# Kernel optimization log

Hardware: AMD Instinct MI355X
Metric: run time of the kernel (lower is better)

## Reference

```python
import jax, jax.numpy as jnp
import numpy as np

B, S, D = 4, 2048, 768
H = 12
HD = D // H
SCALE = HD ** -0.5


def setup_inputs() -> dict:
    key = jax.random.key(0)
    ks = jax.random.split(key, 5)
    std = D ** -0.5
    return {
        "hidden_states": jax.random.normal(ks[0], (B, S, D), dtype=jnp.float32),
        "qkv_w": jax.random.normal(ks[1], (3 * D, D), dtype=jnp.float32) * std,
        "qkv_b": jnp.zeros((3 * D,), dtype=jnp.float32),
        "proj_w": jax.random.normal(ks[2], (D, D), dtype=jnp.float32) * std,
        "proj_b": jnp.zeros((D,), dtype=jnp.float32),
    }


def reference(hidden_states, qkv_w, qkv_b, proj_w, proj_b):
    b, s, d = hidden_states.shape
    # fused QKV projection: [b,s,3d] -> [3,b,H,s,hd]
    mixed = hidden_states @ qkv_w.T + qkv_b
    mixed = mixed.reshape(b, s, 3, H, HD).transpose(2, 0, 3, 1, 4)
    q, k, v = mixed[0], mixed[1], mixed[2]
    # naive attention: full [b,H,s,s] score matrix, as in original module
    scores = jnp.einsum("bhqd,bhkd->bhqk", q, k) * SCALE
    probs = jax.nn.softmax(scores, axis=-1)
    ctx = jnp.einsum("bhqk,bhkd->bhqd", probs, v)
    ctx = ctx.transpose(0, 2, 1, 3).reshape(b, s, d)
    out = ctx @ proj_w.T + proj_b
    return out
```

## Files before the change

### kernel.cpp

```cpp
#include <hip/hip_runtime.h>
#include <hip/hip_bf16.h>

using short8   = __attribute__((ext_vector_type(8))) short;
using floatx4  = __attribute__((ext_vector_type(4))) float;
using floatx16 = __attribute__((ext_vector_type(16))) float;

#define KDIM 768
#define QSCALE 0.18033688011112042f
#define N1 (8192 * 768)
#define N2 (2304 * 768)
#define N3 (768 * 768)

__device__ __forceinline__ short f2bf(float f) {
    union { float f; unsigned u; } v; v.f = f;
    unsigned r = v.u + 0x7fffu + ((v.u >> 16) & 1u);
    return (short)(r >> 16);
}

__device__ __forceinline__ unsigned pack2bf(float a, float b) {
    __hip_bfloat162 h = __float22bfloat162_rn(float2{a, b});
    union { __hip_bfloat162 h; unsigned u; } c; c.h = h;
    return c.u;
}

__device__ __forceinline__ float fast_exp2(float x) {
#if __has_builtin(__builtin_amdgcn_exp2f)
    return __builtin_amdgcn_exp2f(x);
#else
    return exp2f(x);
#endif
}

__device__ __forceinline__ void async16(const void* g, void* l) {
    __builtin_amdgcn_global_load_lds((const __attribute__((address_space(1))) void*)g,
                                     (__attribute__((address_space(3))) void*)l, 16, 0, 0);
}

__global__ void cvt_all(const float* __restrict__ a, const float* __restrict__ b,
                        const float* __restrict__ c, short* __restrict__ oa,
                        short* __restrict__ ob, short* __restrict__ oc) {
    int i = (blockIdx.x * blockDim.x + threadIdx.x) * 4;
    const float* src; short* dst;
    if (i < N1)            { src = a + i;            dst = oa + i; }
    else if (i < N1 + N2)  { src = b + (i - N1);     dst = ob + (i - N1); }
    else if (i < N1+N2+N3) { src = c + (i - N1 - N2); dst = oc + (i - N1 - N2); }
    else return;
    float4 v = *(const float4*)src;
    short4 o;
    o.x = f2bf(v.x); o.y = f2bf(v.y); o.z = f2bf(v.z); o.w = f2bf(v.w);
    *(short4*)dst = o;
}

__global__ __launch_bounds__(256) void gemm_qkv(
    const short* __restrict__ X, const short* __restrict__ W,
    const float* __restrict__ bias,
    short* __restrict__ Qb, short* __restrict__ Kb, short* __restrict__ Vb)
{
    __shared__ short As[128 * 32];
    __shared__ short Bs[128 * 32];
    int tid = threadIdx.x;
    int w = tid >> 6, l = tid & 63;
    int lane16 = l & 15, quad = l >> 4;
    int wm = w & 1, wn = w >> 1;
    int m0 = blockIdx.y * 128, n0 = blockIdx.x * 128;

    floatx4 acc[4][4] = {};

    int srow = w * 32 + (l >> 2);
    int scol = (l & 3) * 8;
    const short* Xg = X + (size_t)(m0 + srow) * KDIM + scol;
    const short* Wg = W + (size_t)(n0 + srow) * KDIM + scol;
    short* AsW = As + (w * 32) * 32;
    short* BsW = Bs + (w * 32) * 32;

    for (int kb = 0; kb < KDIM; kb += 32) {
        __syncthreads();
        async16(Xg + kb,              AsW);
        async16(Xg + kb + 16 * KDIM,  AsW + 16 * 32);
        async16(Wg + kb,              BsW);
        async16(Wg + kb + 16 * KDIM,  BsW + 16 * 32);
        __syncthreads();
        short8 a[4], b[4];
#pragma unroll
        for (int mt = 0; mt < 4; mt++) a[mt] = *(const short8*)(As + (wm * 64 + mt * 16 + lane16) * 32 + quad * 8);
#pragma unroll
        for (int nt = 0; nt < 4; nt++) b[nt] = *(const short8*)(Bs + (wn * 64 + nt * 16 + lane16) * 32 + quad * 8);
#pragma unroll
        for (int mt = 0; mt < 4; mt++)
#pragma unroll
            for (int nt = 0; nt < 4; nt++)
                acc[mt][nt] = __builtin_amdgcn_mfma_f32_16x16x32_bf16(a[mt], b[nt], acc[mt][nt], 0, 0, 0);
    }

#pragma unroll
    for (int mt = 0; mt < 4; mt++) {
        int row = m0 + wm * 64 + mt * 16 + quad * 4;
#pragma unroll
        for (int nt = 0; nt < 4; nt++) {
            int col = n0 + wn * 64 + nt * 16 + lane16;
            int qkv = (col >= 1536) ? 2 : ((col >= 768) ? 1 : 0);
            int rem = col - qkv * 768;
            int h = rem >> 6, e = rem & 63;
            short* dst = (qkv == 0) ? Qb : ((qkv == 1) ? Kb : Vb);
            float sc = (qkv == 0) ? (float)QSCALE : 1.0f;
            float bv = bias[col];
#pragma unroll
            for (int r = 0; r < 4; r++) {
                int i  = row + r;
                int b_ = i >> 11, s_ = i & 2047;
                dst[(((size_t)(b_ * 12 + h)) * 2048 + s_) * 64 + e] = f2bf((acc[mt][nt][r] + bv) * sc);
            }
        }
    }
}

__global__ __launch_bounds__(256) void transpose_v(
    const short* __restrict__ Vb, short* __restrict__ Vt)
{
    __shared__ short T[64 * 66];
    int tid = threadIdx.x;
    int s0 = blockIdx.x * 64, bh = blockIdx.y;
    const short* src = Vb + (size_t)bh * 2048 * 64;
    short* dst = Vt + (size_t)bh * 64 * 2048;

#pragma unroll
    for (int i = 0; i < 2; i++) {
        int slot = i * 256 + tid;
        int s_loc = slot >> 3, ec = slot & 7;
        short8 v = *(const short8*)(src + (size_t)(s0 + s_loc) * 64 + ec * 8);
        *(short8*)(T + s_loc * 66 + ec * 8) = v;
    }
    __syncthreads();
#pragma unroll
    for (int i = 0; i < 2; i++) {
        int slot = i * 256 + tid;
        int e_loc = slot >> 3, sc = slot & 7;
        short8 o;
#pragma unroll
        for (int j = 0; j < 8; j++) {
            int p = sc * 8 + j;
            int kp = (p & 0x33) | ((p & 4) << 1) | ((p & 8) >> 1);
            o[j] = T[kp * 66 + e_loc];
        }
        *(short8*)(dst + (size_t)e_loc * 2048 + s0 + sc * 8) = o;
    }
}

__global__ __launch_bounds__(256, 3) void attn(
    const short* __restrict__ Qb, const short* __restrict__ Kb,
    const short* __restrict__ Vt, short* __restrict__ Ctx)
{
    __shared__ short Ks[512 * 8];
    __shared__ short Vs[512 * 8];
    int tid = threadIdx.x, w = tid >> 6, l = tid & 63;
    int l32 = l & 31, half = l >> 5;
    int qt = blockIdx.x, bh = blockIdx.y;
    const short* Qh  = Qb + (size_t)bh * 2048 * 64;
    const short* Kh  = Kb + (size_t)bh * 2048 * 64;
    const short* Vth = Vt + (size_t)bh * 64 * 2048;
    int qbase = qt * 128 + w * 32;

    const short* kSrc[2];
    const short* vSrc[2];
    short* kDst[2];
    short* vDst[2];
#pragma unroll
    for (int i = 0; i < 2; i++) {
        int slot = i * 256 + tid;
        int row = slot >> 3;
        int g = (slot & 7) ^ (row & 7);
        kSrc[i] = Kh + (size_t)row * 64 + g * 8;
        vSrc[i] = Vth + (size_t)row * 2048 + g * 8;
        kDst[i] = Ks + (size_t)(i * 256 + w * 64) * 8;
        vDst[i] = Vs + (size_t)(i * 256 + w * 64) * 8;
    }

    short8 qf[4];
#pragma unroll
    for (int ks = 0; ks < 4; ks++)
        qf[ks] = *(const short8*)(Qh + (size_t)(qbase + l32) * 64 + ks * 16 + half * 8);

    float lsum = 0.f;
    floatx16 acc[2] = {};
    int sw = l32 & 7;

    for (int kt = 0; kt < 32; kt++) {
        __syncthreads();
#pragma unroll
        for (int i = 0; i < 2; i++) {
            async16(kSrc[i] + (size_t)kt * 64 * 64, kDst[i]);
            async16(vSrc[i] + (size_t)kt * 64,      vDst[i]);
        }
        __syncthreads();

        floatx16 s[2];
#pragma unroll
        for (int nt = 0; nt < 2; nt++) {
            floatx16 c = {};
            int rowb = (nt * 32 + l32) * 8;
#pragma unroll
            for (int ks = 0; ks < 4; ks++) {
                short8 kf = *(const short8*)(Ks + (size_t)(rowb + ((ks * 2 + half) ^ sw)) * 8);
                c = __builtin_amdgcn_mfma_f32_32x32x16_bf16(kf, qf[ks], c, 0, 0, 0);
            }
            s[nt] = c;
        }

        union { short8 s8; unsigned u[4]; } pa[4];
#pragma unroll
        for (int nt = 0; nt < 2; nt++)
#pragma unroll
            for (int r = 0; r < 16; r += 2) {
                float p0 = fast_exp2(s[nt][r]);
                float p1 = fast_exp2(s[nt][r + 1]);
                lsum += p0 + p1;
                pa[2 * nt + (r >> 3)].u[(r & 7) >> 1] = pack2bf(p0, p1);
            }

#pragma unroll
        for (int nt = 0; nt < 2; nt++) {
            int rowb = (nt * 32 + l32) * 8;
#pragma unroll
            for (int ks = 0; ks < 4; ks++) {
                short8 vf = *(const short8*)(Vs + (size_t)(rowb + ((ks * 2 + half) ^ sw)) * 8);
                acc[nt] = __builtin_amdgcn_mfma_f32_32x32x16_bf16(pa[ks].s8, vf, acc[nt], 0, 0, 0);
            }
        }
    }

    float denom = lsum + __shfl_xor(lsum, 32);
    float inv_self = 1.0f / denom;

    int b_ = bh / 12, h = bh % 12;
#pragma unroll
    for (int nt = 0; nt < 2; nt++)
#pragma unroll
        for (int r = 0; r < 16; r++) {
            int qloc = (r & 3) + 8 * (r >> 2) + 4 * half;
            float invq = __shfl(inv_self, qloc);
            int q = qbase + qloc;
            int e = nt * 32 + l32;
            Ctx[((size_t)(b_ * 2048 + q)) * 768 + h * 64 + e] = f2bf(acc[nt][r] * invq);
        }
}

__global__ __launch_bounds__(256) void gemm_out(
    const short* __restrict__ Ctx, const short* __restrict__ W,
    const float* __restrict__ bias, float* __restrict__ out)
{
    __shared__ short As[128 * 32];
    __shared__ short Bs[128 * 32];
    int tid = threadIdx.x;
    int w = tid >> 6, l = tid & 63;
    int lane16 = l & 15, quad = l >> 4;
    int wm = w & 1, wn = w >> 1;
    int m0 = blockIdx.y * 128, n0 = blockIdx.x * 128;

    floatx4 acc[4][4] = {};

    int srow = w * 32 + (l >> 2);
    int scol = (l & 3) * 8;
    const short* Xg = Ctx + (size_t)(m0 + srow) * KDIM + scol;
    const short* Wg = W + (size_t)(n0 + srow) * KDIM + scol;
    short* AsW = As + (w * 32) * 32;
    short* BsW = Bs + (w * 32) * 32;

    for (int kb = 0; kb < KDIM; kb += 32) {
        __syncthreads();
        async16(Xg + kb,             AsW);
        async16(Xg + kb + 16 * KDIM, AsW + 16 * 32);
        async16(Wg + kb,             BsW);
        async16(Wg + kb + 16 * KDIM, BsW + 16 * 32);
        __syncthreads();
        short8 a[4], b[4];
#pragma unroll
        for (int mt = 0; mt < 4; mt++) a[mt] = *(const short8*)(As + (wm * 64 + mt * 16 + lane16) * 32 + quad * 8);
#pragma unroll
        for (int nt = 0; nt < 4; nt++) b[nt] = *(const short8*)(Bs + (wn * 64 + nt * 16 + lane16) * 32 + quad * 8);
#pragma unroll
        for (int mt = 0; mt < 4; mt++)
#pragma unroll
            for (int nt = 0; nt < 4; nt++)
                acc[mt][nt] = __builtin_amdgcn_mfma_f32_16x16x32_bf16(a[mt], b[nt], acc[mt][nt], 0, 0, 0);
    }

#pragma unroll
    for (int mt = 0; mt < 4; mt++) {
        int row = m0 + wm * 64 + mt * 16 + quad * 4;
#pragma unroll
        for (int nt = 0; nt < 4; nt++) {
            int col = n0 + wn * 64 + nt * 16 + lane16;
            float bv = bias[col];
#pragma unroll
            for (int r = 0; r < 4; r++)
                out[(size_t)(row + r) * 768 + col] = acc[mt][nt][r] + bv;
        }
    }
}

extern "C" void kernel_launch(void* const* d_in, const int* in_sizes, int n_in,
                              void* d_out, int out_size, void* d_ws, size_t ws_size,
                              hipStream_t stream) {
    const float* hs     = (const float*)d_in[0];
    const float* qkv_w  = (const float*)d_in[1];
    const float* qkv_b  = (const float*)d_in[2];
    const float* proj_w = (const float*)d_in[3];
    const float* proj_b = (const float*)d_in[4];
    float* out = (float*)d_out;

    short* Xb  = (short*)d_ws;
    short* W1b = Xb  + (size_t)8192 * 768;
    short* W2b = W1b + (size_t)2304 * 768;
    short* Qb  = W2b + (size_t)768 * 768;
    short* Kb  = Qb  + (size_t)8192 * 768;
    short* Vb  = Kb  + (size_t)8192 * 768;
    short* Ctx = Vb  + (size_t)8192 * 768;
    short* Vt  = Xb;

    int ntot = (N1 + N2 + N3) / 4;
    cvt_all<<<(ntot + 255) / 256, 256, 0, stream>>>(hs, qkv_w, proj_w, Xb, W1b, W2b);

    gemm_qkv<<<dim3(18, 64), 256, 0, stream>>>(Xb, W1b, qkv_b, Qb, Kb, Vb);
    transpose_v<<<dim3(32, 48), 256, 0, stream>>>(Vb, Vt);
    attn<<<dim3(16, 48), 256, 0, stream>>>(Qb, Kb, Vt, Ctx);
    gemm_out<<<dim3(6, 64), 256, 0, stream>>>(Ctx, W2b, proj_b, out);
}
```

Baseline: 221.8 us.

## Fuse V transpose into QKV GEMM epilogue via LDS staging; shrink out-proj tile

The QKV GEMM epilogue now stages each 128x64 output slice in shared memory and writes Q/K rows with coalesced 16-byte stores, while V is written directly in transposed (permuted) layout. This removes the separate transpose_v kernel and its extra global round trip. The scattered 2-byte epilogue stores are also replaced by vector stores. Separately, the output projection GEMM uses 64-row tiles, doubling the grid to 768 blocks for better CU fill, at the cost of less reuse per block.

```diff
diff --git a/kernel.cpp b/kernel.cpp
--- a/kernel.cpp
+++ b/kernel.cpp
@@ -54,10 +54,13 @@
 __global__ __launch_bounds__(256) void gemm_qkv(
     const short* __restrict__ X, const short* __restrict__ W,
     const float* __restrict__ bias,
-    short* __restrict__ Qb, short* __restrict__ Kb, short* __restrict__ Vb)
+    short* __restrict__ Qb, short* __restrict__ Kb, short* __restrict__ Vt)
 {
-    __shared__ short As[128 * 32];
-    __shared__ short Bs[128 * 32];
+    __shared__ __attribute__((aligned(16))) short SMEM[128 * 72];
+    short* As = SMEM;
+    short* Bs = SMEM + 128 * 32;
+    short* T  = SMEM;
+
     int tid = threadIdx.x;
     int w = tid >> 6, l = tid & 63;
     int lane16 = l & 15, quad = l >> 4;
@@ -92,57 +95,57 @@
                 acc[mt][nt] = __builtin_amdgcn_mfma_f32_16x16x32_bf16(a[mt], b[nt], acc[mt][nt], 0, 0, 0);
     }
 
-#pragma unroll
-    for (int mt = 0; mt < 4; mt++) {
-        int row = m0 + wm * 64 + mt * 16 + quad * 4;
-#pragma unroll
-        for (int nt = 0; nt < 4; nt++) {
-            int col = n0 + wn * 64 + nt * 16 + lane16;
-            int qkv = (col >= 1536) ? 2 : ((col >= 768) ? 1 : 0);
-            int rem = col - qkv * 768;
-            int h = rem >> 6, e = rem & 63;
-            short* dst = (qkv == 0) ? Qb : ((qkv == 1) ? Kb : Vb);
-            float sc = (qkv == 0) ? (float)QSCALE : 1.0f;
-            float bv = bias[col];
-#pragma unroll
-            for (int r = 0; r < 4; r++) {
-                int i  = row + r;
-                int b_ = i >> 11, s_ = i & 2047;
-                dst[(((size_t)(b_ * 12 + h)) * 2048 + s_) * 64 + e] = f2bf((acc[mt][nt][r] + bv) * sc);
-            }
-        }
-    }
-}
-
-__global__ __launch_bounds__(256) void transpose_v(
-    const short* __restrict__ Vb, short* __restrict__ Vt)
-{
-    __shared__ short T[64 * 66];
-    int tid = threadIdx.x;
-    int s0 = blockIdx.x * 64, bh = blockIdx.y;
-    const short* src = Vb + (size_t)bh * 2048 * 64;
-    short* dst = Vt + (size_t)bh * 64 * 2048;
-
-#pragma unroll
-    for (int i = 0; i < 2; i++) {
-        int slot = i * 256 + tid;
-        int s_loc = slot >> 3, ec = slot & 7;
-        short8 v = *(const short8*)(src + (size_t)(s0 + s_loc) * 64 + ec * 8);
-        *(short8*)(T + s_loc * 66 + ec * 8) = v;
-    }
-    __syncthreads();
-#pragma unroll
-    for (int i = 0; i < 2; i++) {
-        int slot = i * 256 + tid;
-        int e_loc = slot >> 3, sc = slot & 7;
-        short8 o;
-#pragma unroll
-        for (int j = 0; j < 8; j++) {
-            int p = sc * 8 + j;
-            int kp = (p & 0x33) | ((p & 4) << 1) | ((p & 8) >> 1);
-            o[j] = T[kp * 66 + e_loc];
-        }
-        *(short8*)(dst + (size_t)e_loc * 2048 + s0 + sc * 8) = o;
+    int b_  = m0 >> 11;
+    int m0s = m0 & 2047;
+#pragma unroll
+    for (int g = 0; g < 2; g++) {
+        __syncthreads();
+        if (wn == g) {
+#pragma unroll
+            for (int mt = 0; mt < 4; mt++)
+#pragma unroll
+                for (int nt = 0; nt < 4; nt++) {
+                    int col = n0 + g * 64 + nt * 16 + lane16;
+                    float sc = (col < 768) ? (float)QSCALE : 1.0f;
+                    float bv = bias[col];
+#pragma unroll
+                    for (int r = 0; r < 4; r++) {
+                        int row = wm * 64 + mt * 16 + quad * 4 + r;
+                        T[row * 72 + nt * 16 + lane16] = f2bf((acc[mt][nt][r] + bv) * sc);
+                    }
+                }
+        }
+        __syncthreads();
+        int col0 = n0 + g * 64;
+        int qkv = (col0 >= 1536) ? 2 : ((col0 >= 768) ? 1 : 0);
+        int h = (col0 - qkv * 768) >> 6;
+        size_t bh = (size_t)(b_ * 12 + h);
+        if (qkv < 2) {
+            short* dst = ((qkv == 0) ? Qb : Kb) + bh * 2048 * 64;
+#pragma unroll
+            for (int u = 0; u < 4; u++) {
+                int unit = u * 256 + tid;
+                int row = unit >> 3, c = unit & 7;
+                short8 v = *(const short8*)(T + row * 72 + c * 8);
+                *(short8*)(dst + (size_t)(m0s + row) * 64 + c * 8) = v;
+            }
+        } else {
+            short* dst = Vt + bh * 64 * 2048;
+#pragma unroll
+            for (int u = 0; u < 4; u++) {
+                int unit = u * 256 + tid;
+                int e = unit >> 4, sc_ = unit & 15;
+                short8 o;
+#pragma unroll
+                for (int j = 0; j < 8; j++) {
+                    int pos = sc_ * 8 + j;
+                    int t = pos >> 6, tp = pos & 63;
+                    int kp = (tp & 0x33) | ((tp & 4) << 1) | ((tp & 8) >> 1);
+                    o[j] = T[(t * 64 + kp) * 72 + e];
+                }
+                *(short8*)(dst + (size_t)e * 2048 + m0s + sc_ * 8) = o;
+            }
+        }
     }
 }
 
@@ -248,48 +251,50 @@
     const short* __restrict__ Ctx, const short* __restrict__ W,
     const float* __restrict__ bias, float* __restrict__ out)
 {
-    __shared__ short As[128 * 32];
+    __shared__ short As[64 * 32];
     __shared__ short Bs[128 * 32];
     int tid = threadIdx.x;
     int w = tid >> 6, l = tid & 63;
     int lane16 = l & 15, quad = l >> 4;
-    int wm = w & 1, wn = w >> 1;
-    int m0 = blockIdx.y * 128, n0 = blockIdx.x * 128;
-
-    floatx4 acc[4][4] = {};
-
-    int srow = w * 32 + (l >> 2);
-    int scol = (l & 3) * 8;
-    const short* Xg = Ctx + (size_t)(m0 + srow) * KDIM + scol;
-    const short* Wg = W + (size_t)(n0 + srow) * KDIM + scol;
-    short* AsW = As + (w * 32) * 32;
-    short* BsW = Bs + (w * 32) * 32;
+    int m0 = blockIdx.y * 64, n0 = blockIdx.x * 128;
+
+    floatx4 acc[4][2] = {};
+
+    const short* XgA = Ctx + (size_t)(m0 + (tid >> 2)) * KDIM + (tid & 3) * 8;
+    short* AsD = As + (size_t)(w * 64) * 8;
+    const short* XgB[2];
+    short* BsD[2];
+#pragma unroll
+    for (int i = 0; i < 2; i++) {
+        int unit = i * 256 + tid;
+        XgB[i] = W + (size_t)(n0 + (unit >> 2)) * KDIM + (unit & 3) * 8;
+        BsD[i] = Bs + (size_t)(i * 256 + w * 64) * 8;
+    }
 
     for (int kb = 0; kb < KDIM; kb += 32) {
         __syncthreads();
-        async16(Xg + kb,             AsW);
-        async16(Xg + kb + 16 * KDIM, AsW + 16 * 32);
-        async16(Wg + kb,             BsW);
-        async16(Wg + kb + 16 * KDIM, BsW + 16 * 32);
-        __syncthreads();
-        short8 a[4], b[4];
-#pragma unroll
-        for (int mt = 0; mt < 4; mt++) a[mt] = *(const short8*)(As + (wm * 64 + mt * 16 + lane16) * 32 + quad * 8);
-#pragma unroll
-        for (int nt = 0; nt < 4; nt++) b[nt] = *(const short8*)(Bs + (wn * 64 + nt * 16 + lane16) * 32 + quad * 8);
+        async16(XgA + kb, AsD);
+        async16(XgB[0] + kb, BsD[0]);
+        async16(XgB[1] + kb, BsD[1]);
+        __syncthreads();
+        short8 a[4], b[2];
+#pragma unroll
+        for (int mt = 0; mt < 4; mt++) a[mt] = *(const short8*)(As + (mt * 16 + lane16) * 32 + quad * 8);
+#pragma unroll
+        for (int nt = 0; nt < 2; nt++) b[nt] = *(const short8*)(Bs + (w * 32 + nt * 16 + lane16) * 32 + quad * 8);
 #pragma unroll
         for (int mt = 0; mt < 4; mt++)
 #pragma unroll
-            for (int nt = 0; nt < 4; nt++)
+            for (int nt = 0; nt < 2; nt++)
                 acc[mt][nt] = __builtin_amdgcn_mfma_f32_16x16x32_bf16(a[mt], b[nt], acc[mt][nt], 0, 0, 0);
     }
 
 #pragma unroll
     for (int mt = 0; mt < 4; mt++) {
-        int row = m0 + wm * 64 + mt * 16 + quad * 4;
-#pragma unroll
-        for (int nt = 0; nt < 4; nt++) {
-            int col = n0 + wn * 64 + nt * 16 + lane16;
+        int row = m0 + mt * 16 + quad * 4;
+#pragma unroll
+        for (int nt = 0; nt < 2; nt++) {
+            int col = n0 + w * 32 + nt * 16 + lane16;
             float bv = bias[col];
 #pragma unroll
             for (int r = 0; r < 4; r++)
@@ -313,15 +318,13 @@
     short* W2b = W1b + (size_t)2304 * 768;
     short* Qb  = W2b + (size_t)768 * 768;
     short* Kb  = Qb  + (size_t)8192 * 768;
-    short* Vb  = Kb  + (size_t)8192 * 768;
-    short* Ctx = Vb  + (size_t)8192 * 768;
-    short* Vt  = Xb;
+    short* Vt  = Kb  + (size_t)8192 * 768;
+    short* Ctx = Vt  + (size_t)8192 * 768;
 
     int ntot = (N1 + N2 + N3) / 4;
     cvt_all<<<(ntot + 255) / 256, 256, 0, stream>>>(hs, qkv_w, proj_w, Xb, W1b, W2b);
 
-    gemm_qkv<<<dim3(18, 64), 256, 0, stream>>>(Xb, W1b, qkv_b, Qb, Kb, Vb);
-    transpose_v<<<dim3(32, 48), 256, 0, stream>>>(Vb, Vt);
+    gemm_qkv<<<dim3(18, 64), 256, 0, stream>>>(Xb, W1b, qkv_b, Qb, Kb, Vt);
     attn<<<dim3(16, 48), 256, 0, stream>>>(Qb, Kb, Vt, Ctx);
-    gemm_out<<<dim3(6, 64), 256, 0, stream>>>(Ctx, W2b, proj_b, out);
-}
+    gemm_out<<<dim3(6, 128), 256, 0, stream>>>(Ctx, W2b, proj_b, out);
+}
```

Result: slower. 232.5 us (+4.8%).

## Double-buffer K/V tiles in attention and shrink output GEMM tile

Applied to the files above, without the earlier changes.

The attention kernel now keeps two LDS buffers for K and V and issues the async loads for the next key tile before computing on the current one, removing the second barrier per iteration so loads overlap with MFMA work. LDS use per block doubles, which may limit occupancy at the requested three blocks per CU. Separately, the output projection GEMM moves from 128x128 to 64x128 tiles with each wave owning a 64x32 slab. This doubles the grid to 768 blocks for better CU fill, at the cost of less operand reuse per block.

```diff
diff --git a/kernel.cpp b/kernel.cpp
--- a/kernel.cpp
+++ b/kernel.cpp
@@ -150,8 +150,8 @@
     const short* __restrict__ Qb, const short* __restrict__ Kb,
     const short* __restrict__ Vt, short* __restrict__ Ctx)
 {
-    __shared__ short Ks[512 * 8];
-    __shared__ short Vs[512 * 8];
+    __shared__ short Ks[2][512 * 8];
+    __shared__ short Vs[2][512 * 8];
     int tid = threadIdx.x, w = tid >> 6, l = tid & 63;
     int l32 = l & 31, half = l >> 5;
     int qt = blockIdx.x, bh = blockIdx.y;
@@ -162,8 +162,8 @@
 
     const short* kSrc[2];
     const short* vSrc[2];
-    short* kDst[2];
-    short* vDst[2];
+    short* kDst[2][2];
+    short* vDst[2][2];
 #pragma unroll
     for (int i = 0; i < 2; i++) {
         int slot = i * 256 + tid;
@@ -171,8 +171,11 @@
         int g = (slot & 7) ^ (row & 7);
         kSrc[i] = Kh + (size_t)row * 64 + g * 8;
         vSrc[i] = Vth + (size_t)row * 2048 + g * 8;
-        kDst[i] = Ks + (size_t)(i * 256 + w * 64) * 8;
-        vDst[i] = Vs + (size_t)(i * 256 + w * 64) * 8;
+#pragma unroll
+        for (int b = 0; b < 2; b++) {
+            kDst[b][i] = &Ks[b][(size_t)(i * 256 + w * 64) * 8];
+            vDst[b][i] = &Vs[b][(size_t)(i * 256 + w * 64) * 8];
+        }
     }
 
     short8 qf[4];
@@ -184,14 +187,25 @@
     floatx16 acc[2] = {};
     int sw = l32 & 7;
 
+#pragma unroll
+    for (int i = 0; i < 2; i++) {
+        async16(kSrc[i], kDst[0][i]);
+        async16(vSrc[i], vDst[0][i]);
+    }
+
     for (int kt = 0; kt < 32; kt++) {
         __syncthreads();
-#pragma unroll
-        for (int i = 0; i < 2; i++) {
-            async16(kSrc[i] + (size_t)kt * 64 * 64, kDst[i]);
-            async16(vSrc[i] + (size_t)kt * 64,      vDst[i]);
-        }
-        __syncthreads();
+        int b = kt & 1;
+        if (kt < 31) {
+            int nb = b ^ 1;
+#pragma unroll
+            for (int i = 0; i < 2; i++) {
+                async16(kSrc[i] + (size_t)(kt + 1) * 64 * 64, kDst[nb][i]);
+                async16(vSrc[i] + (size_t)(kt + 1) * 64,      vDst[nb][i]);
+            }
+        }
+        const short* KsB = Ks[b];
+        const short* VsB = Vs[b];
 
         floatx16 s[2];
 #pragma unroll
@@ -200,7 +214,7 @@
             int rowb = (nt * 32 + l32) * 8;
 #pragma unroll
             for (int ks = 0; ks < 4; ks++) {
-                short8 kf = *(const short8*)(Ks + (size_t)(rowb + ((ks * 2 + half) ^ sw)) * 8);
+                short8 kf = *(const short8*)(KsB + (size_t)(rowb + ((ks * 2 + half) ^ sw)) * 8);
                 c = __builtin_amdgcn_mfma_f32_32x32x16_bf16(kf, qf[ks], c, 0, 0, 0);
             }
             s[nt] = c;
@@ -222,7 +236,7 @@
             int rowb = (nt * 32 + l32) * 8;
 #pragma unroll
             for (int ks = 0; ks < 4; ks++) {
-                short8 vf = *(const short8*)(Vs + (size_t)(rowb + ((ks * 2 + half) ^ sw)) * 8);
+                short8 vf = *(const short8*)(VsB + (size_t)(rowb + ((ks * 2 + half) ^ sw)) * 8);
                 acc[nt] = __builtin_amdgcn_mfma_f32_32x32x16_bf16(pa[ks].s8, vf, acc[nt], 0, 0, 0);
             }
         }
@@ -248,48 +262,50 @@
     const short* __restrict__ Ctx, const short* __restrict__ W,
     const float* __restrict__ bias, float* __restrict__ out)
 {
-    __shared__ short As[128 * 32];
+    __shared__ short As[64 * 32];
     __shared__ short Bs[128 * 32];
     int tid = threadIdx.x;
     int w = tid >> 6, l = tid & 63;
     int lane16 = l & 15, quad = l >> 4;
-    int wm = w & 1, wn = w >> 1;
-    int m0 = blockIdx.y * 128, n0 = blockIdx.x * 128;
-
-    floatx4 acc[4][4] = {};
-
-    int srow = w * 32 + (l >> 2);
-    int scol = (l & 3) * 8;
-    const short* Xg = Ctx + (size_t)(m0 + srow) * KDIM + scol;
-    const short* Wg = W + (size_t)(n0 + srow) * KDIM + scol;
-    short* AsW = As + (w * 32) * 32;
-    short* BsW = Bs + (w * 32) * 32;
+    int m0 = blockIdx.y * 64, n0 = blockIdx.x * 128;
+
+    floatx4 acc[4][2] = {};
+
+    const short* XgA = Ctx + (size_t)(m0 + (tid >> 2)) * KDIM + (tid & 3) * 8;
+    short* AsD = As + (size_t)(w * 64) * 8;
+    const short* XgB[2];
+    short* BsD[2];
+#pragma unroll
+    for (int i = 0; i < 2; i++) {
+        int unit = i * 256 + tid;
+        XgB[i] = W + (size_t)(n0 + (unit >> 2)) * KDIM + (unit & 3) * 8;
+        BsD[i] = Bs + (size_t)(i * 256 + w * 64) * 8;
+    }
 
     for (int kb = 0; kb < KDIM; kb += 32) {
         __syncthreads();
-        async16(Xg + kb,             AsW);
-        async16(Xg + kb + 16 * KDIM, AsW + 16 * 32);
-        async16(Wg + kb,             BsW);
-        async16(Wg + kb + 16 * KDIM, BsW + 16 * 32);
-        __syncthreads();
-        short8 a[4], b[4];
-#pragma unroll
-        for (int mt = 0; mt < 4; mt++) a[mt] = *(const short8*)(As + (wm * 64 + mt * 16 + lane16) * 32 + quad * 8);
-#pragma unroll
-        for (int nt = 0; nt < 4; nt++) b[nt] = *(const short8*)(Bs + (wn * 64 + nt * 16 + lane16) * 32 + quad * 8);
+        async16(XgA + kb, AsD);
+        async16(XgB[0] + kb, BsD[0]);
+        async16(XgB[1] + kb, BsD[1]);
+        __syncthreads();
+        short8 a[4], b[2];
+#pragma unroll
+        for (int mt = 0; mt < 4; mt++) a[mt] = *(const short8*)(As + (mt * 16 + lane16) * 32 + quad * 8);
+#pragma unroll
+        for (int nt = 0; nt < 2; nt++) b[nt] = *(const short8*)(Bs + (w * 32 + nt * 16 + lane16) * 32 + quad * 8);
 #pragma unroll
         for (int mt = 0; mt < 4; mt++)
 #pragma unroll
-            for (int nt = 0; nt < 4; nt++)
+            for (int nt = 0; nt < 2; nt++)
                 acc[mt][nt] = __builtin_amdgcn_mfma_f32_16x16x32_bf16(a[mt], b[nt], acc[mt][nt], 0, 0, 0);
     }
 
 #pragma unroll
     for (int mt = 0; mt < 4; mt++) {
-        int row = m0 + wm * 64 + mt * 16 + quad * 4;
-#pragma unroll
-        for (int nt = 0; nt < 4; nt++) {
-            int col = n0 + wn * 64 + nt * 16 + lane16;
+        int row = m0 + mt * 16 + quad * 4;
+#pragma unroll
+        for (int nt = 0; nt < 2; nt++) {
+            int col = n0 + w * 32 + nt * 16 + lane16;
             float bv = bias[col];
 #pragma unroll
             for (int r = 0; r < 4; r++)
@@ -323,5 +339,5 @@
     gemm_qkv<<<dim3(18, 64), 256, 0, stream>>>(Xb, W1b, qkv_b, Qb, Kb, Vb);
     transpose_v<<<dim3(32, 48), 256, 0, stream>>>(Vb, Vt);
     attn<<<dim3(16, 48), 256, 0, stream>>>(Qb, Kb, Vt, Ctx);
-    gemm_out<<<dim3(6, 64), 256, 0, stream>>>(Ctx, W2b, proj_b, out);
-}
+    gemm_out<<<dim3(6, 128), 256, 0, stream>>>(Ctx, W2b, proj_b, out);
+}
```

Measured after the change: 235.8 us. 6.3% more time.
